# Kernel tuning notes

Measured on AMD Instinct MI355X. Metric: run time of the kernel, lower is better.

## Reference

```python
import jax, jax.numpy as jnp
from jax import lax
import numpy as np

N, E = 10000, 120000
IN_DIM = 128
HID = 32        # hidden_dim
HEADS = 8
OUT = 32        # out_dim
HD = HID * HEADS  # 256
EPS = 1e-5


def _bn(x, g, b):
    # BatchNorm1d (training-mode batch stats, deterministic reference)
    mu = x.mean(0)
    var = x.var(0)
    return g * (x - mu) * lax.rsqrt(var + EPS) + b


def _seg_softmax(logits, seg, n):
    # softmax over edges grouped by destination node, per head
    m = jax.ops.segment_max(logits, seg, num_segments=n)
    ex = jnp.exp(logits - m[seg])
    s = jax.ops.segment_sum(ex, seg, num_segments=n)
    return ex / (s[seg] + 1e-16)


def _gat_layer(h, src, dst, fc_w, a_l, a_r, bn_g, bn_b, heads, out, residual):
    n = h.shape[0]
    h_in = h
    feat = (h @ fc_w).reshape(n, heads, out)      # [N,H,D]
    el = (feat * a_l).sum(-1)                     # [N,H]
    er = (feat * a_r).sum(-1)
    logits = jax.nn.leaky_relu(el[src] + er[dst], 0.2)  # [E,H]
    alpha = _seg_softmax(logits, dst, n)
    rst = jax.ops.segment_sum(alpha[..., None] * feat[src], dst, num_segments=n)
    rst = rst.reshape(n, heads * out)
    rst = _bn(rst, bn_g, bn_b)
    rst = jax.nn.elu(rst)
    if residual:
        rst = h_in + rst
    return rst


def setup_inputs():
    key = jax.random.key(0)
    ks = jax.random.split(key, 20)
    s = 0.02
    d = {}
    d["h"] = jax.random.normal(ks[0], (N, IN_DIM), jnp.float32)
    d["e"] = jax.random.normal(ks[1], (E, IN_DIM), jnp.float32)
    d["src"] = jax.random.randint(ks[2], (E,), 0, N, jnp.int32)
    d["dst"] = jax.random.randint(ks[3], (E,), 0, N, jnp.int32)
    d["W_emb"] = jax.random.normal(ks[4], (IN_DIM, HD)) * s
    d["b_emb"] = jnp.zeros((HD,))
    d["W_p1"] = jax.random.normal(ks[5], (IN_DIM, HID * HID)) * s
    d["b_p1"] = jnp.zeros((HID * HID,))
    d["W_p2"] = jax.random.normal(ks[6], (IN_DIM, HID)) * s
    d["b_p2"] = jnp.zeros((HID,))
    d["W_conv"] = jax.random.normal(ks[7], (1, 2, 3)) * s  # Conv1d(2->1,k=3)
    d["b_conv"] = jnp.zeros((1,))
    d["W_ep2"] = jax.random.normal(ks[8], (IN_DIM, HD)) * s
    d["b_ep2"] = jnp.zeros((HD,))
    d["W_ep3"] = jax.random.normal(ks[9], (HID, HD)) * s
    d["b_ep3"] = jnp.zeros((HD,))
    d["bn_g"] = jnp.ones((HD,))
    d["bn_b"] = jnp.zeros((HD,))
    d["fc1"] = jax.random.normal(ks[10], (HD, HD)) * s
    d["al1"] = jax.random.normal(ks[11], (HEADS, HID)) * s
    d["ar1"] = jax.random.normal(ks[12], (HEADS, HID)) * s
    d["g1"] = jnp.ones((HD,))
    d["b1"] = jnp.zeros((HD,))
    d["fc2"] = jax.random.normal(ks[13], (HD, OUT)) * s
    d["al2"] = jax.random.normal(ks[14], (1, OUT)) * s
    d["ar2"] = jax.random.normal(ks[15], (1, OUT)) * s
    d["g2"] = jnp.ones((OUT,))
    d["b2"] = jnp.zeros((OUT,))
    return d


def reference(h, e, src, dst, W_emb, b_emb, W_p1, b_p1, W_p2, b_p2,
              W_conv, b_conv, W_ep2, b_ep2, W_ep3, b_ep3, bn_g, bn_b,
              fc1, al1, ar1, g1, b1, fc2, al2, ar2, g2, b2):
    # local edge feature: Conv1d over stacked (src,dst) node feats
    edge = jnp.stack([h[src], h[dst]], axis=1)  # [E,2,IN_DIM]
    conv = lax.conv_general_dilated(edge, W_conv, (1,), [(1, 1)],
                                    dimension_numbers=("NCH", "OIH", "NCH"))
    lr_local = conv[:, 0, :] + b_conv[0]         # [E,IN_DIM]
    lr_e_local = lr_local @ W_ep2 + b_ep2        # [E,HD]
    # low-rank global affinity: mm[i,j,k] = sum_d p1[i,k,d]*p2[j,d],
    # gathered only at edges (same math as the dense NxNxHID tensor)
    p1 = (h @ W_p1 + b_p1).reshape(-1, HID, HID)  # [N,HID,HID]
    p2 = h @ W_p2 + b_p2                          # [N,HID]
    lr_glob = jnp.einsum("ekd,ed->ek", p1[src], p2[dst])  # [E,HID]
    lr_e_global = lr_glob @ W_ep3 + b_ep3        # [E,HD]
    e_feat = jax.nn.relu(_bn(lr_e_local + lr_e_global, bn_g, bn_b))
    del e_feat  # default 'dgl' GATLayer ignores e; kept for faithfulness of math
    hh = h @ W_emb + b_emb                       # embedding_h
    hh = _gat_layer(hh, src, dst, fc1, al1, ar1, g1, b1, HEADS, HID, True)
    hh = _gat_layer(hh, src, dst, fc2, al2, ar2, g2, b2, 1, OUT, False)
    return hh
```

## Files before the change

### kernel.cpp

```cpp
#include <hip/hip_runtime.h>
#include <hip/hip_bf16.h>
#include <math.h>


#define HDIM 256
#define NHEADS 8
#define ODIM 32

typedef unsigned short u16;
typedef __attribute__((ext_vector_type(8))) short short8;
typedef __attribute__((ext_vector_type(4))) float f32x4;

__device__ __forceinline__ float bf2f(u16 u) { return __uint_as_float(((unsigned)u) << 16); }
__device__ __forceinline__ u16 f2bf(float f) {
    unsigned x = __float_as_uint(f);
    return (u16)((x + 0x7FFFu + ((x >> 16) & 1u)) >> 16);
}

__global__ __launch_bounds__(256) void prep_kernel(const float* __restrict__ in_h, const float* __restrict__ W_emb,
                                                   const float* __restrict__ fc1, const float* __restrict__ fc2,
                                                   const int* __restrict__ dstv, int* __restrict__ deg,
                                                   u16* __restrict__ Ah, u16* __restrict__ Bemb,
                                                   u16* __restrict__ Bfc1, u16* __restrict__ Bfc2,
                                                   int n4, int E, int N) {
    int job = blockIdx.y;
    int idx = blockIdx.x * 256 + threadIdx.x;
    if (job == 0) {
        if (idx >= n4) return;
        float4 v = ((const float4*)in_h)[idx];
        ushort4 o = {f2bf(v.x), f2bf(v.y), f2bf(v.z), f2bf(v.w)};
        ((ushort4*)Ah)[idx] = o;
        return;
    }
    if (job == 4) {
        if (idx < E) {
            unsigned d = (unsigned)dstv[idx];
            if (d < (unsigned)N) atomicAdd(&deg[d], 1);
        }
        return;
    }
    const float* B;
    u16* O;
    int K, NC;
    if (job == 1) { B = W_emb; O = Bemb; K = 128; NC = 256; }
    else if (job == 2) { B = fc1; O = Bfc1; K = 256; NC = 256; }
    else { B = fc2; O = Bfc2; K = 256; NC = 32; }
    int KB = K / 32;
    int TOT = (NC / 16) * KB * 64;
    if (idx >= TOT) return;
    int lane = idx & 63;
    int kb = (idx >> 6) % KB;
    int ct = (idx >> 6) / KB;
    int n = ct * 16 + (lane & 15);
    int k0 = kb * 32 + (lane >> 4) * 8;
    u16* dst = O + (size_t)idx * 8;
#pragma unroll
    for (int j = 0; j < 8; j++) dst[j] = f2bf(B[(size_t)(k0 + j) * NC + n]);
}

__global__ __launch_bounds__(256) void scan_kernel(const int* __restrict__ deg, int* __restrict__ offs,
                                                   int* __restrict__ cursor, int n) {
    __shared__ int wsum[4];
    int t = threadIdx.x;
    int chunk = (n + 255) / 256;
    int lo = t * chunk, hi = lo + chunk;
    if (hi > n) hi = n;
    if (lo > n) lo = n;
    int s = 0;
    for (int i = lo; i < hi; i++) s += deg[i];
    int v = s;
#pragma unroll
    for (int d = 1; d < 64; d <<= 1) {
        int nb = __shfl_up(v, d, 64);
        if ((t & 63) >= d) v += nb;
    }
    if ((t & 63) == 63) wsum[t >> 6] = v;
    __syncthreads();
    int woff = 0;
#pragma unroll
    for (int w = 0; w < 4; w++)
        if (w < (t >> 6)) woff += wsum[w];
    int run = woff + v - s;
    for (int i = lo; i < hi; i++) {
        offs[i] = run;
        cursor[i] = run;
        run += deg[i];
    }
    if (t == 255) offs[n] = run;
}

__global__ __launch_bounds__(256) void fill_kernel(const int* __restrict__ src, const int* __restrict__ dstv,
                                                   int* __restrict__ cursor, int* __restrict__ srcs, int E, int N) {
    int i = blockIdx.x * 256 + threadIdx.x;
    if (i < E) {
        unsigned d = (unsigned)dstv[i];
        if (d < (unsigned)N) {
            int p = atomicAdd(&cursor[d], 1);
            if ((unsigned)p < (unsigned)E) srcs[p] = src[i];
        }
    }
}

__global__ __launch_bounds__(256) void fused_emb_fc1(const u16* __restrict__ Ah, const u16* __restrict__ Bemb,
                                                     const float* __restrict__ bemb, const u16* __restrict__ Bfc1,
                                                     const float* __restrict__ al, const float* __restrict__ ar,
                                                     u16* __restrict__ hh, u16* __restrict__ feat1,
                                                     u16* __restrict__ el, u16* __restrict__ er, int M) {
    __shared__ u16 tile[16 * 256];
    const int t = threadIdx.x;
    const int lane = t & 63, w = t >> 6;
    const int rb = (int)blockIdx.x * 16;
    const int m = lane & 15, q = lane >> 4;
    const int arow = rb + m;

    short8 a0[4];
#pragma unroll
    for (int kb = 0; kb < 4; kb++) {
        if (arow < M) a0[kb] = *(const short8*)(Ah + (size_t)arow * 128 + kb * 32 + q * 8);
        else a0[kb] = (short8){0, 0, 0, 0, 0, 0, 0, 0};
    }
    const short8* B8 = (const short8*)Bemb;
#pragma unroll
    for (int ct2 = 0; ct2 < 4; ct2++) {
        const int ct = w * 4 + ct2;
        f32x4 acc = {0.f, 0.f, 0.f, 0.f};
#pragma unroll
        for (int kb = 0; kb < 4; kb++)
            acc = __builtin_amdgcn_mfma_f32_16x16x32_bf16(a0[kb], B8[(ct * 4 + kb) * 64 + lane], acc, 0, 0, 0);
        float bv = bemb[ct * 16 + m];
#pragma unroll
        for (int r = 0; r < 4; r++) {
            int rl = q * 4 + r;
            int ro = rb + rl;
            u16 hv = 0;
            if (ro < M) {
                hv = f2bf(acc[r] + bv);
                hh[(size_t)ro * 256 + ct * 16 + m] = hv;
            }
            int byte = rl * 512 + (ct * 16 + m) * 2;
            tile[(byte ^ ((rl & 7) << 4)) >> 1] = hv;
        }
    }
    __syncthreads();

    short8 af[8];
    {
        int rl = m;
#pragma unroll
        for (int kb = 0; kb < 8; kb++) {
            int byte = rl * 512 + kb * 64 + q * 16;
            af[kb] = *(const short8*)(tile + ((byte ^ ((rl & 7) << 4)) >> 1));
        }
    }
    __syncthreads();

    const short8* Bf = (const short8*)Bfc1;
#pragma unroll
    for (int ct2 = 0; ct2 < 4; ct2++) {
        const int ct = w * 4 + ct2;
        f32x4 acc = {0.f, 0.f, 0.f, 0.f};
#pragma unroll
        for (int kb = 0; kb < 8; kb++)
            acc = __builtin_amdgcn_mfma_f32_16x16x32_bf16(af[kb], Bf[(ct * 8 + kb) * 64 + lane], acc, 0, 0, 0);
#pragma unroll
        for (int r = 0; r < 4; r++) {
            int rl = q * 4 + r;
            int ro = rb + rl;
            u16 v = 0;
            if (ro < M) {
                v = f2bf(acc[r]);
                feat1[(size_t)ro * 256 + ct * 16 + m] = v;
            }
            tile[rl * 256 + ct * 16 + m] = v;
        }
    }
    __syncthreads();

    if (t < 128) {
        int nl = t >> 3, h2 = t & 7;
        int node = rb + nl;
        if (node < M) {
            float a_ = 0.f, b_ = 0.f;
#pragma unroll
            for (int d = 0; d < 32; d++) {
                float fv = bf2f(tile[nl * 256 + h2 * 32 + d]);
                a_ += fv * al[h2 * 32 + d];
                b_ += fv * ar[h2 * 32 + d];
            }
            el[node * 8 + h2] = f2bf(a_);
            er[node * 8 + h2] = f2bf(b_);
        }
    }
}

__device__ __forceinline__ float edgew(float l) {
    l = (l > 0.f) ? l : 0.2f * l;
    l = fminf(fmaxf(l, -30.f), 30.f);
    return __expf(l);
}

__global__ __launch_bounds__(256) void agg1_fused(const u16* __restrict__ feat, const u16* __restrict__ el,
                                                  const u16* __restrict__ er, const int* __restrict__ offs,
                                                  const int* __restrict__ srcs, u16* __restrict__ rst, int N, int E) {
    const int node = blockIdx.x * 4 + (threadIdx.x >> 6);
    const int lane = threadIdx.x & 63;
    if (node >= N) return;
    const int h = lane >> 3;
    int beg = offs[node], end = offs[node + 1];
    if (beg < 0) beg = 0;
    if (end > E) end = E;
    float ern = bf2f(er[node * 8 + h]);
    float ax = 0.f, ay = 0.f, az = 0.f, aw = 0.f, sw = 0.f;
    int j = beg;
    int end4 = beg + ((end - beg) & ~3);
    for (; j < end4; j += 4) {
        int s0 = srcs[j], s1 = srcs[j + 1], s2 = srcs[j + 2], s3 = srcs[j + 3];
        unsigned c0 = (unsigned)s0 < (unsigned)N, c1 = (unsigned)s1 < (unsigned)N;
        unsigned c2 = (unsigned)s2 < (unsigned)N, c3 = (unsigned)s3 < (unsigned)N;
        s0 = c0 ? s0 : 0; s1 = c1 ? s1 : 0; s2 = c2 ? s2 : 0; s3 = c3 ? s3 : 0;
        u16 e0 = el[s0 * 8 + h], e1 = el[s1 * 8 + h], e2 = el[s2 * 8 + h], e3 = el[s3 * 8 + h];
        ushort4 f0 = *(const ushort4*)(feat + (size_t)s0 * 256 + lane * 4);
        ushort4 f1 = *(const ushort4*)(feat + (size_t)s1 * 256 + lane * 4);
        ushort4 f2 = *(const ushort4*)(feat + (size_t)s2 * 256 + lane * 4);
        ushort4 f3 = *(const ushort4*)(feat + (size_t)s3 * 256 + lane * 4);
        float w0 = c0 ? edgew(bf2f(e0) + ern) : 0.f;
        float w1 = c1 ? edgew(bf2f(e1) + ern) : 0.f;
        float w2 = c2 ? edgew(bf2f(e2) + ern) : 0.f;
        float w3 = c3 ? edgew(bf2f(e3) + ern) : 0.f;
        sw += w0 + w1 + w2 + w3;
        ax += w0 * bf2f(f0.x) + w1 * bf2f(f1.x) + w2 * bf2f(f2.x) + w3 * bf2f(f3.x);
        ay += w0 * bf2f(f0.y) + w1 * bf2f(f1.y) + w2 * bf2f(f2.y) + w3 * bf2f(f3.y);
        az += w0 * bf2f(f0.z) + w1 * bf2f(f1.z) + w2 * bf2f(f2.z) + w3 * bf2f(f3.z);
        aw += w0 * bf2f(f0.w) + w1 * bf2f(f1.w) + w2 * bf2f(f2.w) + w3 * bf2f(f3.w);
    }
    for (; j < end; j++) {
        int s = srcs[j];
        if ((unsigned)s >= (unsigned)N) continue;
        float wv = edgew(bf2f(el[s * 8 + h]) + ern);
        ushort4 f4 = *(const ushort4*)(feat + (size_t)s * 256 + lane * 4);
        sw += wv;
        ax += wv * bf2f(f4.x);
        ay += wv * bf2f(f4.y);
        az += wv * bf2f(f4.z);
        aw += wv * bf2f(f4.w);
    }
    float inv = 1.f / (sw + 1e-16f);
    ushort4 o;
    o.x = f2bf(ax * inv); o.y = f2bf(ay * inv); o.z = f2bf(az * inv); o.w = f2bf(aw * inv);
    *(ushort4*)(rst + (size_t)node * 256 + lane * 4) = o;
}

__global__ __launch_bounds__(256) void bn_stats256(const u16* __restrict__ X, float* __restrict__ stats,
                                                   int rows, int RPB) {
    int t = threadIdx.x;
    int rbeg = blockIdx.x * RPB;
    int rend = rbeg + RPB;
    if (rend > rows) rend = rows;
    float s = 0.f, s2 = 0.f;
    for (int r = rbeg; r < rend; r++) {
        float x = bf2f(X[(long)r * 256 + t]);
        s += x;
        s2 += x * x;
    }
    atomicAdd(&stats[t], s);
    atomicAdd(&stats[256 + t], s2);
}

__global__ __launch_bounds__(256) void bn_stats32(const float* __restrict__ X, float* __restrict__ stats,
                                                  int rows, int RPB) {
    __shared__ float ss[256], ss2[256];
    int t = threadIdx.x, c = t & 31, rs = t >> 5;
    int rbeg = blockIdx.x * RPB;
    int rend = rbeg + RPB;
    if (rend > rows) rend = rows;
    float s = 0.f, s2 = 0.f;
    for (int r = rbeg + rs; r < rend; r += 8) {
        float x = X[(long)r * 32 + c];
        s += x;
        s2 += x * x;
    }
    ss[t] = s;
    ss2[t] = s2;
    __syncthreads();
    if (t < 32) {
        for (int j = 32; j < 256; j += 32) { s += ss[t + j]; s2 += ss2[t + j]; }
        atomicAdd(&stats[c], s);
        atomicAdd(&stats[32 + c], s2);
    }
}

__global__ __launch_bounds__(256) void gemm_fc2_fused(const u16* __restrict__ rst, const u16* __restrict__ hh,
                                                      const float* __restrict__ stats, const float* __restrict__ g,
                                                      const float* __restrict__ b, const u16* __restrict__ Bsw,
                                                      const float* __restrict__ al2, const float* __restrict__ ar2,
                                                      float* __restrict__ feat2, float* __restrict__ el2,
                                                      float* __restrict__ er2, int M, float invN) {
    __shared__ float sc[256], sh[256];
    __shared__ float tile[64][32];
    const int t = threadIdx.x;
    {
        float mu = stats[t] * invN;
        float var = fmaxf(stats[256 + t] * invN - mu * mu, 0.f);
        float s = g[t] * rsqrtf(var + 1e-5f);
        sc[t] = s;
        sh[t] = b[t] - mu * s;
    }
    __syncthreads();
    const int lane = t & 63, wq = t >> 6;
    const int rb = blockIdx.x * 64;
    const int m = lane & 15, q = lane >> 4;
    const int row = rb + wq * 16 + m;
    short8 a[8];
#pragma unroll
    for (int kb = 0; kb < 8; kb++) {
        if (row < M) {
            int k0 = kb * 32 + q * 8;
            ushort4 r01 = *(const ushort4*)(rst + (size_t)row * 256 + k0);
            ushort4 r23 = *(const ushort4*)(rst + (size_t)row * 256 + k0 + 4);
            ushort4 h01 = *(const ushort4*)(hh + (size_t)row * 256 + k0);
            ushort4 h23 = *(const ushort4*)(hh + (size_t)row * 256 + k0 + 4);
            u16 rv[8] = {r01.x, r01.y, r01.z, r01.w, r23.x, r23.y, r23.z, r23.w};
            u16 hv[8] = {h01.x, h01.y, h01.z, h01.w, h23.x, h23.y, h23.z, h23.w};
            short8 av;
#pragma unroll
            for (int j = 0; j < 8; j++) {
                int c = k0 + j;
                float y = sc[c] * bf2f(rv[j]) + sh[c];
                y = (y > 0.f) ? y : expm1f(y);
                av[j] = (short)f2bf(bf2f(hv[j]) + y);
            }
            a[kb] = av;
        } else a[kb] = (short8){0, 0, 0, 0, 0, 0, 0, 0};
    }
    const short8* B8 = (const short8*)Bsw;
#pragma unroll
    for (int ct = 0; ct < 2; ct++) {
        f32x4 acc = {0.f, 0.f, 0.f, 0.f};
#pragma unroll
        for (int kb = 0; kb < 8; kb++)
            acc = __builtin_amdgcn_mfma_f32_16x16x32_bf16(a[kb], B8[(ct * 8 + kb) * 64 + lane], acc, 0, 0, 0);
#pragma unroll
        for (int r = 0; r < 4; r++) {
            int rl = wq * 16 + q * 4 + r;
            int ro = rb + rl;
            float v = 0.f;
            if (ro < M) {
                v = acc[r];
                feat2[(size_t)ro * 32 + ct * 16 + m] = v;
            }
            tile[rl][ct * 16 + m] = v;
        }
    }
    __syncthreads();
    if (t < 64) {
        int node = rb + t;
        if (node < M) {
            float a_ = 0.f, b_ = 0.f;
#pragma unroll
            for (int d = 0; d < 32; d++) {
                float fv = tile[t][d];
                a_ += fv * al2[d];
                b_ += fv * ar2[d];
            }
            el2[node] = a_;
            er2[node] = b_;
        }
    }
}

__global__ __launch_bounds__(256) void agg2_fused(const float* __restrict__ feat, const float* __restrict__ el,
                                                  const float* __restrict__ er, const int* __restrict__ offs,
                                                  const int* __restrict__ srcs, float* __restrict__ rst,
                                                  int N, int E) {
    const int t = threadIdx.x;
    const int node = blockIdx.x * 8 + (t >> 5);
    const int d = t & 31;
    if (node >= N) return;
    int beg = offs[node], end = offs[node + 1];
    if (beg < 0) beg = 0;
    if (end > E) end = E;
    float ern = er[node];
    float acc = 0.f, sw = 0.f;
#pragma unroll 2
    for (int j = beg; j < end; j++) {
        int s = srcs[j];
        if ((unsigned)s >= (unsigned)N) continue;
        float wv = edgew(el[s] + ern);
        sw += wv;
        acc += wv * feat[(size_t)s * 32 + d];
    }
    rst[(size_t)node * 32 + d] = acc / (sw + 1e-16f);
}

__global__ __launch_bounds__(256) void bn_apply2(const float* __restrict__ rst, const float* __restrict__ stats,
                                                 const float* __restrict__ g, const float* __restrict__ b,
                                                 float* __restrict__ out, int total, float invN) {
    int idx = blockIdx.x * 256 + threadIdx.x;
    if (idx >= total) return;
    int c = idx & 31;
    float mu = stats[c] * invN;
    float var = fmaxf(stats[32 + c] * invN - mu * mu, 0.f);
    float y = g[c] * (rst[idx] - mu) * rsqrtf(var + 1e-5f) + b[c];
    y = (y > 0.f) ? y : expm1f(y);
    out[idx] = y;
}

extern "C" void kernel_launch(void* const* d_in, const int* in_sizes, int n_in, void* d_out, int out_size, void* d_ws,
                              size_t ws_size, hipStream_t stream) {
    const int N = out_size / ODIM;
    const int E = in_sizes[2];

    const int* src = (const int*)d_in[2];
    const int* dst = (const int*)d_in[3];
    const float* in_h = (const float*)d_in[0];
    const float* W_emb = (const float*)d_in[4];  const float* b_emb = (const float*)d_in[5];
    const float* fc1 = (const float*)d_in[18];   const float* al1 = (const float*)d_in[19];
    const float* ar1 = (const float*)d_in[20];
    const float* g1 = (const float*)d_in[21];    const float* b1 = (const float*)d_in[22];
    const float* fc2 = (const float*)d_in[23];   const float* al2 = (const float*)d_in[24];
    const float* ar2 = (const float*)d_in[25];
    const float* g2 = (const float*)d_in[26];    const float* b2 = (const float*)d_in[27];
    float* out = (float*)d_out;

    char* base = (char*)d_ws;
    size_t off = 0;
    auto alloc = [&](size_t bytes) { void* p = base + off; off += (bytes + 63) & ~63ull; return p; };
    char* zb   = (char*)alloc((size_t)N * 4 + 512 * 4 + 64 * 4);
    int* deg   = (int*)zb;
    float* stats  = (float*)(zb + (size_t)N * 4);
    float* stats2 = stats + 512;
    int* offs  = (int*)alloc((size_t)(N + 1) * 4);
    int* cursor = (int*)alloc((size_t)N * 4);
    int* srcs  = (int*)alloc((size_t)E * 4);
    u16* Ah    = (u16*)alloc((size_t)N * 128 * 2);
    u16* Bemb  = (u16*)alloc((size_t)128 * 256 * 2);
    u16* Bfc1  = (u16*)alloc((size_t)256 * 256 * 2);
    u16* Bfc2  = (u16*)alloc((size_t)256 * 32 * 2);
    u16* hh    = (u16*)alloc((size_t)N * HDIM * 2);
    u16* feat1 = (u16*)alloc((size_t)N * HDIM * 2);
    u16* el1   = (u16*)alloc((size_t)N * 8 * 2);
    u16* er1   = (u16*)alloc((size_t)N * 8 * 2);
    u16* rst   = (u16*)alloc((size_t)N * HDIM * 2);
    float* feat2 = (float*)alloc((size_t)N * 32 * 4);
    float* el2 = (float*)alloc((size_t)N * 4);
    float* er2 = (float*)alloc((size_t)N * 4);
    float* rst2 = (float*)alloc((size_t)N * 32 * 4);

    const int NB16 = (N + 15) / 16;
    const int NB64 = (N + 63) / 64;

    hipMemsetAsync(zb, 0, (size_t)N * 4 + 512 * 4 + 64 * 4, stream);
    prep_kernel<<<dim3((N * 128 / 4 + 255) / 256, 5), 256, 0, stream>>>(in_h, W_emb, fc1, fc2, dst, deg,
                                                                        Ah, Bemb, Bfc1, Bfc2, N * 128 / 4, E, N);
    scan_kernel<<<1, 256, 0, stream>>>(deg, offs, cursor, N);
    fill_kernel<<<(E + 255) / 256, 256, 0, stream>>>(src, dst, cursor, srcs, E, N);
    fused_emb_fc1<<<NB16, 256, 0, stream>>>(Ah, Bemb, b_emb, Bfc1, al1, ar1, hh, feat1, el1, er1, N);
    agg1_fused<<<(N + 3) / 4, 256, 0, stream>>>(feat1, el1, er1, offs, srcs, rst, N, E);
    bn_stats256<<<(N + 39) / 40, 256, 0, stream>>>(rst, stats, N, 40);
    gemm_fc2_fused<<<NB64, 256, 0, stream>>>(rst, hh, stats, g1, b1, Bfc2, al2, ar2, feat2, el2, er2, N, 1.f / N);
    agg2_fused<<<(N + 7) / 8, 256, 0, stream>>>(feat2, el2, er2, offs, srcs, rst2, N, E);
    bn_stats32<<<(N + 63) / 64, 256, 0, stream>>>(rst2, stats2, N, 64);
    bn_apply2<<<(N * ODIM + 255) / 256, 256, 0, stream>>>(rst2, stats2, g2, b2, out, N * ODIM, 1.f / N);
}
```

Baseline: 259.4 us.

## Merge CSR fill into emb/fc1 launch and split fc2 GEMM K across waves

The CSR fill step, which scatters edge sources via atomics, now runs as extra blocks of the fused embedding/fc1 kernel, so one launch is removed and the fill can overlap the GEMM blocks. The fc2 GEMM now has each block handle 16 rows instead of 64. Its four waves are split over two column tiles and two K halves, with partial sums reduced through shared memory. This gives four times as many blocks for better occupancy on a small GEMM, in exchange for an extra barrier and more blocks re-reading B and recomputing the BN scale and shift.

```diff
diff --git a/kernel.cpp b/kernel.cpp
--- a/kernel.cpp
+++ b/kernel.cpp
@@ -89,23 +89,25 @@
     if (t == 255) offs[n] = run;
 }
 
-__global__ __launch_bounds__(256) void fill_kernel(const int* __restrict__ src, const int* __restrict__ dstv,
-                                                   int* __restrict__ cursor, int* __restrict__ srcs, int E, int N) {
-    int i = blockIdx.x * 256 + threadIdx.x;
-    if (i < E) {
-        unsigned d = (unsigned)dstv[i];
-        if (d < (unsigned)N) {
-            int p = atomicAdd(&cursor[d], 1);
-            if ((unsigned)p < (unsigned)E) srcs[p] = src[i];
-        }
-    }
-}
-
 __global__ __launch_bounds__(256) void fused_emb_fc1(const u16* __restrict__ Ah, const u16* __restrict__ Bemb,
                                                      const float* __restrict__ bemb, const u16* __restrict__ Bfc1,
                                                      const float* __restrict__ al, const float* __restrict__ ar,
                                                      u16* __restrict__ hh, u16* __restrict__ feat1,
-                                                     u16* __restrict__ el, u16* __restrict__ er, int M) {
+                                                     u16* __restrict__ el, u16* __restrict__ er,
+                                                     const int* __restrict__ src, const int* __restrict__ dstv,
+                                                     int* __restrict__ cursor, int* __restrict__ srcs,
+                                                     int M, int NB, int E, int N) {
+    if ((int)blockIdx.x >= NB) {
+        int i = ((int)blockIdx.x - NB) * 256 + (int)threadIdx.x;
+        if (i < E) {
+            unsigned d = (unsigned)dstv[i];
+            if (d < (unsigned)N) {
+                int p = atomicAdd(&cursor[d], 1);
+                if ((unsigned)p < (unsigned)E) srcs[p] = src[i];
+            }
+        }
+        return;
+    }
     __shared__ u16 tile[16 * 256];
     const int t = threadIdx.x;
     const int lane = t & 63, w = t >> 6;
@@ -296,7 +298,8 @@
                                                       float* __restrict__ feat2, float* __restrict__ el2,
                                                       float* __restrict__ er2, int M, float invN) {
     __shared__ float sc[256], sh[256];
-    __shared__ float tile[64][32];
+    __shared__ float red[2][256];
+    __shared__ float tile[16][32];
     const int t = threadIdx.x;
     {
         float mu = stats[t] * invN;
@@ -306,15 +309,16 @@
         sh[t] = b[t] - mu * s;
     }
     __syncthreads();
-    const int lane = t & 63, wq = t >> 6;
-    const int rb = blockIdx.x * 64;
+    const int lane = t & 63, w = t >> 6;
+    const int ct = w & 1, kh = w >> 1;
+    const int rb = (int)blockIdx.x * 16;
     const int m = lane & 15, q = lane >> 4;
-    const int row = rb + wq * 16 + m;
-    short8 a[8];
-#pragma unroll
-    for (int kb = 0; kb < 8; kb++) {
+    const int row = rb + m;
+    short8 a[4];
+#pragma unroll
+    for (int j = 0; j < 4; j++) {
         if (row < M) {
-            int k0 = kb * 32 + q * 8;
+            int k0 = (kh * 4 + j) * 32 + q * 8;
             ushort4 r01 = *(const ushort4*)(rst + (size_t)row * 256 + k0);
             ushort4 r23 = *(const ushort4*)(rst + (size_t)row * 256 + k0 + 4);
             ushort4 h01 = *(const ushort4*)(hh + (size_t)row * 256 + k0);
@@ -323,36 +327,38 @@
             u16 hv[8] = {h01.x, h01.y, h01.z, h01.w, h23.x, h23.y, h23.z, h23.w};
             short8 av;
 #pragma unroll
-            for (int j = 0; j < 8; j++) {
-                int c = k0 + j;
-                float y = sc[c] * bf2f(rv[j]) + sh[c];
+            for (int jj = 0; jj < 8; jj++) {
+                int c = k0 + jj;
+                float y = sc[c] * bf2f(rv[jj]) + sh[c];
                 y = (y > 0.f) ? y : expm1f(y);
-                av[j] = (short)f2bf(bf2f(hv[j]) + y);
-            }
-            a[kb] = av;
-        } else a[kb] = (short8){0, 0, 0, 0, 0, 0, 0, 0};
+                av[jj] = (short)f2bf(bf2f(hv[jj]) + y);
+            }
+            a[j] = av;
+        } else a[j] = (short8){0, 0, 0, 0, 0, 0, 0, 0};
     }
     const short8* B8 = (const short8*)Bsw;
-#pragma unroll
-    for (int ct = 0; ct < 2; ct++) {
-        f32x4 acc = {0.f, 0.f, 0.f, 0.f};
-#pragma unroll
-        for (int kb = 0; kb < 8; kb++)
-            acc = __builtin_amdgcn_mfma_f32_16x16x32_bf16(a[kb], B8[(ct * 8 + kb) * 64 + lane], acc, 0, 0, 0);
+    f32x4 acc = {0.f, 0.f, 0.f, 0.f};
+#pragma unroll
+    for (int j = 0; j < 4; j++)
+        acc = __builtin_amdgcn_mfma_f32_16x16x32_bf16(a[j], B8[(ct * 8 + kh * 4 + j) * 64 + lane], acc, 0, 0, 0);
+    if (kh == 1) *(f32x4*)&red[ct][lane * 4] = acc;
+    __syncthreads();
+    if (kh == 0) {
+        f32x4 p = *(const f32x4*)&red[ct][lane * 4];
 #pragma unroll
         for (int r = 0; r < 4; r++) {
-            int rl = wq * 16 + q * 4 + r;
+            int rl = q * 4 + r;
             int ro = rb + rl;
             float v = 0.f;
             if (ro < M) {
-                v = acc[r];
+                v = acc[r] + p[r];
                 feat2[(size_t)ro * 32 + ct * 16 + m] = v;
             }
             tile[rl][ct * 16 + m] = v;
         }
     }
     __syncthreads();
-    if (t < 64) {
+    if (t < 16) {
         int node = rb + t;
         if (node < M) {
             float a_ = 0.f, b_ = 0.f;
@@ -447,17 +453,17 @@
     float* rst2 = (float*)alloc((size_t)N * 32 * 4);
 
     const int NB16 = (N + 15) / 16;
-    const int NB64 = (N + 63) / 64;
+    const int NBF = (E + 255) / 256;
 
     hipMemsetAsync(zb, 0, (size_t)N * 4 + 512 * 4 + 64 * 4, stream);
     prep_kernel<<<dim3((N * 128 / 4 + 255) / 256, 5), 256, 0, stream>>>(in_h, W_emb, fc1, fc2, dst, deg,
                                                                         Ah, Bemb, Bfc1, Bfc2, N * 128 / 4, E, N);
     scan_kernel<<<1, 256, 0, stream>>>(deg, offs, cursor, N);
-    fill_kernel<<<(E + 255) / 256, 256, 0, stream>>>(src, dst, cursor, srcs, E, N);
-    fused_emb_fc1<<<NB16, 256, 0, stream>>>(Ah, Bemb, b_emb, Bfc1, al1, ar1, hh, feat1, el1, er1, N);
+    fused_emb_fc1<<<NB16 + NBF, 256, 0, stream>>>(Ah, Bemb, b_emb, Bfc1, al1, ar1, hh, feat1, el1, er1,
+                                                  src, dst, cursor, srcs, N, NB16, E, N);
     agg1_fused<<<(N + 3) / 4, 256, 0, stream>>>(feat1, el1, er1, offs, srcs, rst, N, E);
     bn_stats256<<<(N + 39) / 40, 256, 0, stream>>>(rst, stats, N, 40);
-    gemm_fc2_fused<<<NB64, 256, 0, stream>>>(rst, hh, stats, g1, b1, Bfc2, al2, ar2, feat2, el2, er2, N, 1.f / N);
+    gemm_fc2_fused<<<NB16, 256, 0, stream>>>(rst, hh, stats, g1, b1, Bfc2, al2, ar2, feat2, el2, er2, N, 1.f / N);
     agg2_fused<<<(N + 7) / 8, 256, 0, stream>>>(feat2, el2, er2, offs, srcs, rst2, N, E);
     bn_stats32<<<(N + 63) / 64, 256, 0, stream>>>(rst2, stats2, N, 64);
     bn_apply2<<<(N * ODIM + 255) / 256, 256, 0, stream>>>(rst2, stats2, g2, b2, out, N * ODIM, 1.f / N);
```

After: 252.0 us. 2.9% less time.
